# Kernel tuning notes

Hardware: AMD Instinct MI355X
Metric: run time of the kernel (lower is better)

## Reference

```python
import jax, jax.numpy as jnp
import numpy as np

NUM_NODES = 1024
NUM_HEADS = 8
HIDDEN = 256
BOND_DIM = 64
NUM_LAYERS = 3


def _build_edge_index(n):
    # ring + chord graph, both directions -> 4n directed edges, no duplicate (src,tgt) pairs
    u = np.arange(n)
    src = np.concatenate([u, u, (u + 1) % n, (u + 2) % n])
    dst = np.concatenate([(u + 1) % n, (u + 2) % n, u, u])
    return jnp.asarray(np.stack([src, dst]), dtype=jnp.int32)


def setup_inputs() -> dict:
    key = jax.random.key(0)
    ks = jax.random.split(key, 16)
    H, L, B = HIDDEN, NUM_LAYERS, BOND_DIM
    E = 4 * NUM_NODES
    s = 0.02
    inp = {
        "edge_index": _build_edge_index(NUM_NODES),
        "bond_features": jax.random.normal(ks[0], (E, B), jnp.float32),
        # bond_embedding Linear + W_h Linear (stored as [in, out])
        "W_emb": jax.random.normal(ks[1], (B, H), jnp.float32) * s,
        "b_emb": jnp.zeros((H,), jnp.float32),
        "W_h": jax.random.normal(ks[2], (H, H), jnp.float32) * s,
        "b_h": jnp.zeros((H,), jnp.float32),
        # per-layer attention block: pre-LN, qkv in-proj, out-proj
        "ln1_g": jnp.ones((L, H), jnp.float32),
        "ln1_b": jnp.zeros((L, H), jnp.float32),
        "in_w": jax.random.normal(ks[3], (L, H, 3 * H), jnp.float32) * s,
        "in_b": jnp.zeros((L, 3 * H), jnp.float32),
        "out_w": jax.random.normal(ks[4], (L, H, H), jnp.float32) * s,
        "out_b": jnp.zeros((L, H), jnp.float32),
        # per-layer bond_update: Linear -> LayerNorm -> GELU
        "up_w": jax.random.normal(ks[5], (L, H, H), jnp.float32) * s,
        "up_b": jnp.zeros((L, H), jnp.float32),
        "ln2_g": jnp.ones((L, H), jnp.float32),
        "ln2_b": jnp.zeros((L, H), jnp.float32),
    }
    return inp


def _layer_norm(x, g, b, eps=1e-5):
    m = jnp.mean(x, axis=-1, keepdims=True)
    v = jnp.var(x, axis=-1, keepdims=True)
    return (x - m) * jax.lax.rsqrt(v + eps) * g + b


def _mha(x, in_w, in_b, out_w, out_b):
    # x: [E, H]; standard torch MultiheadAttention (batch of 1)
    E, H = x.shape
    d = H // NUM_HEADS
    qkv = x @ in_w + in_b                                  # [E, 3H]
    q, k, v = jnp.split(qkv, 3, axis=-1)
    q = q.reshape(E, NUM_HEADS, d).transpose(1, 0, 2)       # [h, E, d]
    k = k.reshape(E, NUM_HEADS, d).transpose(1, 0, 2)
    v = v.reshape(E, NUM_HEADS, d).transpose(1, 0, 2)
    scores = jnp.einsum("hqd,hkd->hqk", q, k) / jnp.sqrt(jnp.float32(d))
    p = jax.nn.softmax(scores, axis=-1)
    o = jnp.einsum("hqk,hkd->hqd", p, v)                    # [h, E, d]
    o = o.transpose(1, 0, 2).reshape(E, H)
    return o @ out_w + out_b


def _bond_aggregation(edge_index, h):
    # r_e = sum_{e' : tgt(e')=tgt(e), src(e')!=src(e)} (h[e'] - h[e])
    # with no duplicate (src,tgt) pairs this is S[tgt] - deg[tgt] * h
    tgt = edge_index[1]
    S = jax.ops.segment_sum(h, tgt, num_segments=NUM_NODES)                 # [N, H]
    deg = jax.ops.segment_sum(jnp.ones(h.shape[:1], h.dtype), tgt, num_segments=NUM_NODES)
    return S[tgt] - deg[tgt][:, None] * h


def reference(edge_index, bond_features, W_emb, b_emb, W_h, b_h,
              ln1_g, ln1_b, in_w, in_b, out_w, out_b,
              up_w, up_b, ln2_g, ln2_b):
    h = jax.nn.gelu(bond_features @ W_emb + b_emb, approximate=False)
    h = h @ W_h + b_h
    for t in range(NUM_LAYERS):
        r = _bond_aggregation(edge_index, h)
        xn = _layer_norm(r, ln1_g[t], ln1_b[t])
        attn = _mha(xn, in_w[t], in_b[t], out_w[t], out_b[t])
        # block output = attn + r (residual inside block), forward adds + r again
        t_ij = attn + r + r
        u = t_ij @ up_w[t] + up_b[t]
        h = jax.nn.gelu(_layer_norm(u, ln2_g[t], ln2_b[t]), approximate=False)
    return h
```

## Files before the change

### kernel.cpp

```cpp
#include <hip/hip_runtime.h>
#include <hip/hip_bf16.h>
#include <math.h>

#define N_NODES 1024
#define NE      4096
#define HDIM    256
#define QSCALE  0.2550348634f

typedef __hip_bfloat16 bf16;
typedef __attribute__((ext_vector_type(8))) short bf16x8;
typedef __attribute__((ext_vector_type(4))) float f32x4;

__device__ __forceinline__ float u2f(unsigned short u) {
  return __uint_as_float(((unsigned)u) << 16);
}
__device__ __forceinline__ short f2bs(float x) {
  unsigned u = __float_as_uint(x);
  unsigned r = u + 0x7FFFu + ((u >> 16) & 1u);
  return (short)(r >> 16);
}
__device__ __forceinline__ float gelu_f(float x) {
  return 0.5f * x * (1.0f + erff(x * 0.70710678118654752f));
}
__device__ __forceinline__ short rdbf(const void* p, int i, int flag) {
  return flag ? ((const short*)p)[i] : f2bs(((const float*)p)[i]);
}
__device__ __forceinline__ float fexp2(float x) {
#if __has_builtin(__builtin_amdgcn_exp2f)
  return __builtin_amdgcn_exp2f(x);
#else
  return exp2f(x);
#endif
}
__device__ __forceinline__ unsigned pk2(float lo, float hi) {
  return (__float_as_uint(hi) & 0xFFFF0000u) | (__float_as_uint(lo) >> 16);
}
__device__ __forceinline__ unsigned pk2r(float lo, float hi) {
  return (unsigned)(unsigned short)f2bs(lo) |
         ((unsigned)(unsigned short)f2bs(hi) << 16);
}

__global__ __launch_bounds__(64) void k_detect(const unsigned* __restrict__ w,
                                               int* __restrict__ flag) {
  int t = threadIdx.x;
  int cnt = 0;
  for (int i = 0; i < 16; ++i) {
    unsigned v = w[t * 16 + i];
    unsigned e = (v >> 7) & 0xFFu;
    cnt += (e >= 100u && e <= 132u) ? 1 : 0;
  }
#pragma unroll
  for (int k = 1; k < 64; k <<= 1) cnt += __shfl_xor(cnt, k, 64);
  if (t == 0) *flag = (cnt > 512) ? 1 : 0;
}

struct WPtrs { const void* w_emb; const void* w_h; const void* in_w;
               const void* out_w; const void* up_w; };
__global__ __launch_bounds__(256) void k_prep_w(WPtrs a, short* __restrict__ Wt,
                                                const int* __restrict__ flag) {
  int i = blockIdx.x * 256 + threadIdx.x;
  if (i >= 1064960) return;
  const int fl = *flag;
  if (i < 16384) {
    int k = i >> 8, n = i & 255;
    Wt[n * 64 + k] = rdbf(a.w_emb, i, fl);
  } else if (i < 81920) {
    int j = i - 16384;
    int k = j >> 8, n = j & 255;
    Wt[16384 + n * 256 + k] = rdbf(a.w_h, j, fl);
  } else if (i < 671744) {
    int j = i - 81920;
    int t = j / 196608, jj = j % 196608;
    int k = jj / 768, n = jj % 768;
    Wt[81920 + t * 196608 + n * 256 + k] = rdbf(a.in_w, j, fl);
  } else if (i < 868352) {
    int j = i - 671744;
    int t = j >> 16, jj = j & 65535;
    int k = jj >> 8, n = jj & 255;
    Wt[671744 + t * 65536 + n * 256 + k] = rdbf(a.out_w, j, fl);
  } else {
    int j = i - 868352;
    int t = j >> 16, jj = j & 65535;
    int k = jj >> 8, n = jj & 255;
    Wt[868352 + t * 65536 + n * 256 + k] = rdbf(a.up_w, j, fl);
  }
}

struct PPtrs { const void* p[9]; };
__global__ __launch_bounds__(256) void k_cvt_small(PPtrs a, float* __restrict__ dst,
                                                   const int* __restrict__ flag) {
  const int sz[9] = {256, 256, 768, 768, 2304, 768, 768, 768, 768};
  int i = blockIdx.x * 256 + threadIdx.x;
  if (i >= 7424) return;
  int seg = 0, off = i;
  while (off >= sz[seg]) { off -= sz[seg]; ++seg; }
  dst[i] = *flag ? u2f(((const unsigned short*)a.p[seg])[off])
                 : ((const float*)a.p[seg])[off];
}

__global__ __launch_bounds__(256) void k_build_inv(const int* __restrict__ tgt,
                                                   int* __restrict__ cnt,
                                                   int* __restrict__ inv) {
  int e = blockIdx.x * 256 + threadIdx.x;
  if (e < NE) {
    int t = tgt[e];
    int s = atomicAdd(&cnt[t], 1);
    if (s < 8) inv[t * 8 + s] = e;
  }
}

template <int K, bool RAW, bool GELU, bool RES, bool WF, bool WB>
__global__ __launch_bounds__(256) void k_mgemm(const short* __restrict__ A,
                                               const short* __restrict__ Bt,
                                               const float* __restrict__ bias,
                                               const float* __restrict__ res,
                                               float* __restrict__ outF,
                                               short* __restrict__ outB,
                                               const int* __restrict__ flag,
                                               int M, int N) {
  __shared__ alignas(16) short As[64 * K];
  __shared__ alignas(16) short Bs[64 * K];
  const int tid = threadIdx.x;
  const int wave = tid >> 6, lane = tid & 63;
  const int m = lane & 15, quad = lane >> 4;
  const int bm = blockIdx.x * 64, bn = blockIdx.y * 64;
  const int m0 = (wave & 1) * 32, n0 = (wave >> 1) * 32;

  constexpr int CPR = K >> 3;
  constexpr int CPT = K >> 5;

  const int fl = RAW ? *flag : 1;

  int4 ra[CPT], rb[CPT];
#pragma unroll
  for (int i = 0; i < CPT; ++i) {
    const int c = tid + (i << 8);
    const int row = c / CPR, kc = c % CPR;
    if (RAW && !fl) {
      const float* af = (const float*)A + (size_t)(bm + row) * K + kc * 8;
      unsigned* vu = (unsigned*)&ra[i];
      vu[0] = pk2r(af[0], af[1]);
      vu[1] = pk2r(af[2], af[3]);
      vu[2] = pk2r(af[4], af[5]);
      vu[3] = pk2r(af[6], af[7]);
    } else {
      ra[i] = *(const int4*)(A + (size_t)(bm + row) * K + kc * 8);
    }
    rb[i] = *(const int4*)(Bt + (size_t)(bn + row) * K + kc * 8);
  }
#pragma unroll
  for (int i = 0; i < CPT; ++i) {
    const int c = tid + (i << 8);
    const int row = c / CPR, kc = c % CPR;
    *(int4*)&As[row * K + ((kc ^ (row & 7)) << 3)] = ra[i];
    *(int4*)&Bs[row * K + ((kc ^ (row & 7)) << 3)] = rb[i];
  }
  __syncthreads();

  f32x4 acc[2][2];
  acc[0][0] = acc[0][1] = acc[1][0] = acc[1][1] = (f32x4){0.f, 0.f, 0.f, 0.f};

  const int sw = m & 7;
#pragma unroll
  for (int ks = 0; ks < K / 32; ++ks) {
    const int ca = ((ks * 4 + quad) ^ sw) << 3;
    bf16x8 a0 = *(const bf16x8*)&As[(m0 + m) * K + ca];
    bf16x8 a1 = *(const bf16x8*)&As[(m0 + 16 + m) * K + ca];
    bf16x8 b0 = *(const bf16x8*)&Bs[(n0 + m) * K + ca];
    bf16x8 b1 = *(const bf16x8*)&Bs[(n0 + 16 + m) * K + ca];
    acc[0][0] = __builtin_amdgcn_mfma_f32_16x16x32_bf16(a0, b0, acc[0][0], 0, 0, 0);
    acc[0][1] = __builtin_amdgcn_mfma_f32_16x16x32_bf16(a0, b1, acc[0][1], 0, 0, 0);
    acc[1][0] = __builtin_amdgcn_mfma_f32_16x16x32_bf16(a1, b0, acc[1][0], 0, 0, 0);
    acc[1][1] = __builtin_amdgcn_mfma_f32_16x16x32_bf16(a1, b1, acc[1][1], 0, 0, 0);
  }

#pragma unroll
  for (int i = 0; i < 2; ++i)
#pragma unroll
    for (int j = 0; j < 2; ++j) {
      const int col = bn + n0 + j * 16 + m;
      const float bv = bias[col];
#pragma unroll
      for (int r = 0; r < 4; ++r) {
        const int row = bm + m0 + i * 16 + quad * 4 + r;
        float v = acc[i][j][r] + bv;
        if (GELU) v = gelu_f(v);
        if (RES) v += 2.0f * res[(size_t)row * N + col];
        if (WF) outF[(size_t)row * N + col] = v;
        if (WB) outB[(size_t)row * N + col] = f2bs(v);
      }
    }
}

__global__ __launch_bounds__(256) void k_mgemm_out(const short* __restrict__ Opart,
                                                   const float* __restrict__ lpart,
                                                   const short* __restrict__ Bt,
                                                   const float* __restrict__ bias,
                                                   const float* __restrict__ res,
                                                   short* __restrict__ outB) {
  constexpr int K = 256;
  __shared__ alignas(16) short As[64 * K];
  __shared__ alignas(16) short Bs[64 * K];
  const int tid = threadIdx.x;
  const int wave = tid >> 6, lane = tid & 63;
  const int m = lane & 15, quad = lane >> 4;
  const int bm = blockIdx.x * 64, bn = blockIdx.y * 64;
  const int m0 = (wave & 1) * 32, n0 = (wave >> 1) * 32;

  int4 ra[8], rb[8];
#pragma unroll
  for (int i = 0; i < 8; ++i) {
    const int c = tid + (i << 8);
    const int row = c >> 5, kc = c & 31;
    const int R = bm + row, head = kc >> 2;
    float o[8] = {0.f, 0.f, 0.f, 0.f, 0.f, 0.f, 0.f, 0.f};
    float l = 0.f;
#pragma unroll
    for (int s = 0; s < 4; ++s) {
      int4 ov = *(const int4*)(Opart + (size_t)s * 1048576 + (size_t)R * 256 + kc * 8);
      const unsigned short* os = (const unsigned short*)&ov;
#pragma unroll
      for (int j = 0; j < 8; ++j) o[j] += u2f(os[j]);
      l += lpart[(size_t)(s * 8 + head) * 4096 + R];
    }
    const float inv = 1.0f / l;
    unsigned* vu = (unsigned*)&ra[i];
    vu[0] = pk2r(o[0] * inv, o[1] * inv);
    vu[1] = pk2r(o[2] * inv, o[3] * inv);
    vu[2] = pk2r(o[4] * inv, o[5] * inv);
    vu[3] = pk2r(o[6] * inv, o[7] * inv);
    rb[i] = *(const int4*)(Bt + (size_t)(bn + row) * K + kc * 8);
  }
#pragma unroll
  for (int i = 0; i < 8; ++i) {
    const int c = tid + (i << 8);
    const int row = c >> 5, kc = c & 31;
    *(int4*)&As[row * K + ((kc ^ (row & 7)) << 3)] = ra[i];
    *(int4*)&Bs[row * K + ((kc ^ (row & 7)) << 3)] = rb[i];
  }
  __syncthreads();

  f32x4 acc[2][2];
  acc[0][0] = acc[0][1] = acc[1][0] = acc[1][1] = (f32x4){0.f, 0.f, 0.f, 0.f};

  const int sw = m & 7;
#pragma unroll
  for (int ks = 0; ks < K / 32; ++ks) {
    const int ca = ((ks * 4 + quad) ^ sw) << 3;
    bf16x8 a0 = *(const bf16x8*)&As[(m0 + m) * K + ca];
    bf16x8 a1 = *(const bf16x8*)&As[(m0 + 16 + m) * K + ca];
    bf16x8 b0 = *(const bf16x8*)&Bs[(n0 + m) * K + ca];
    bf16x8 b1 = *(const bf16x8*)&Bs[(n0 + 16 + m) * K + ca];
    acc[0][0] = __builtin_amdgcn_mfma_f32_16x16x32_bf16(a0, b0, acc[0][0], 0, 0, 0);
    acc[0][1] = __builtin_amdgcn_mfma_f32_16x16x32_bf16(a0, b1, acc[0][1], 0, 0, 0);
    acc[1][0] = __builtin_amdgcn_mfma_f32_16x16x32_bf16(a1, b0, acc[1][0], 0, 0, 0);
    acc[1][1] = __builtin_amdgcn_mfma_f32_16x16x32_bf16(a1, b1, acc[1][1], 0, 0, 0);
  }

#pragma unroll
  for (int i = 0; i < 2; ++i)
#pragma unroll
    for (int j = 0; j < 2; ++j) {
      const int col = bn + n0 + j * 16 + m;
      const float bv = bias[col];
#pragma unroll
      for (int r = 0; r < 4; ++r) {
        const int row = bm + m0 + i * 16 + quad * 4 + r;
        float v = acc[i][j][r] + bv + 2.0f * res[(size_t)row * 256 + col];
        outB[(size_t)row * 256 + col] = f2bs(v);
      }
    }
}

__global__ __launch_bounds__(256) void k_mgemm_qkv(const short* __restrict__ A,
                                                   const short* __restrict__ Bt,
                                                   const float* __restrict__ bias,
                                                   short* __restrict__ Qh,
                                                   short* __restrict__ Kh,
                                                   short* __restrict__ Vt) {
  constexpr int K = 256;
  __shared__ alignas(16) short As[64 * K];
  __shared__ alignas(16) short Bs[64 * K];
  const int tid = threadIdx.x;
  const int wave = tid >> 6, lane = tid & 63;
  const int m = lane & 15, quad = lane >> 4;
  const int bm = blockIdx.x * 64, bn = blockIdx.y * 64;
  const int m0 = (wave & 1) * 32, n0 = (wave >> 1) * 32;

  int4 ra[8], rb[8];
#pragma unroll
  for (int i = 0; i < 8; ++i) {
    const int c = tid + (i << 8);
    const int row = c >> 5, kc = c & 31;
    ra[i] = *(const int4*)(A + (size_t)(bm + row) * K + kc * 8);
    rb[i] = *(const int4*)(Bt + (size_t)(bn + row) * K + kc * 8);
  }
#pragma unroll
  for (int i = 0; i < 8; ++i) {
    const int c = tid + (i << 8);
    const int row = c >> 5, kc = c & 31;
    *(int4*)&As[row * K + ((kc ^ (row & 7)) << 3)] = ra[i];
    *(int4*)&Bs[row * K + ((kc ^ (row & 7)) << 3)] = rb[i];
  }
  __syncthreads();

  f32x4 acc[2][2];
  acc[0][0] = acc[0][1] = acc[1][0] = acc[1][1] = (f32x4){0.f, 0.f, 0.f, 0.f};

  const int sw = m & 7;
#pragma unroll
  for (int ks = 0; ks < K / 32; ++ks) {
    const int ca = ((ks * 4 + quad) ^ sw) << 3;
    bf16x8 a0 = *(const bf16x8*)&As[(m0 + m) * K + ca];
    bf16x8 a1 = *(const bf16x8*)&As[(m0 + 16 + m) * K + ca];
    bf16x8 b0 = *(const bf16x8*)&Bs[(n0 + m) * K + ca];
    bf16x8 b1 = *(const bf16x8*)&Bs[(n0 + 16 + m) * K + ca];
    acc[0][0] = __builtin_amdgcn_mfma_f32_16x16x32_bf16(a0, b0, acc[0][0], 0, 0, 0);
    acc[0][1] = __builtin_amdgcn_mfma_f32_16x16x32_bf16(a0, b1, acc[0][1], 0, 0, 0);
    acc[1][0] = __builtin_amdgcn_mfma_f32_16x16x32_bf16(a1, b0, acc[1][0], 0, 0, 0);
    acc[1][1] = __builtin_amdgcn_mfma_f32_16x16x32_bf16(a1, b1, acc[1][1], 0, 0, 0);
  }

#pragma unroll
  for (int i = 0; i < 2; ++i)
#pragma unroll
    for (int j = 0; j < 2; ++j) {
      const int col = bn + n0 + j * 16 + m;
      const float bv = bias[col];
      const int row0 = bm + m0 + i * 16 + quad * 4;
      if (col < 256) {
        const int head = col >> 5, d = col & 31;
#pragma unroll
        for (int r = 0; r < 4; ++r)
          Qh[(size_t)head * 131072 + (row0 + r) * 32 + d] =
              f2bs((acc[i][j][r] + bv) * QSCALE);
      } else if (col < 512) {
        const int c = col - 256, head = c >> 5, d = c & 31;
#pragma unroll
        for (int r = 0; r < 4; ++r)
          Kh[(size_t)head * 131072 + (row0 + r) * 32 + d] = f2bs(acc[i][j][r] + bv);
      } else {
        const int c = col - 512, head = c >> 5, d = c & 31;
        const int p0 = (row0 & ~63) + ((row0 >> 5) & 1) * 32 +
                       ((row0 >> 2) & 3) * 8 + ((row0 >> 4) & 1) * 4;
        ushort4 w;
        w.x = (unsigned short)f2bs(acc[i][j][0] + bv);
        w.y = (unsigned short)f2bs(acc[i][j][1] + bv);
        w.z = (unsigned short)f2bs(acc[i][j][2] + bv);
        w.w = (unsigned short)f2bs(acc[i][j][3] + bv);
        *(ushort4*)(Vt + (size_t)head * 131072 + d * 4096 + p0) = w;
      }
    }
}

__global__ __launch_bounds__(256) void k_rln2(const int* __restrict__ tgt,
                                              const int* __restrict__ cnt,
                                              const int* __restrict__ inv,
                                              const float* __restrict__ h,
                                              const float* __restrict__ g,
                                              const float* __restrict__ b,
                                              float* __restrict__ r,
                                              short* __restrict__ xnb) {
  __shared__ float red1[4], red2[4];
  const int e = blockIdx.x, d = threadIdx.x;
  const int t = tgt[e];
  const int c = cnt[t];
  float S = 0.f;
  for (int j = 0; j < c; ++j)
    S += h[(size_t)inv[t * 8 + j] * HDIM + d];
  float rv = S - (float)c * h[(size_t)e * HDIM + d];
  r[(size_t)e * HDIM + d] = rv;

  float s = rv;
#pragma unroll
  for (int k = 1; k < 64; k <<= 1) s += __shfl_xor(s, k, 64);
  if ((d & 63) == 0) red1[d >> 6] = s;
  __syncthreads();
  float mean = (red1[0] + red1[1] + red1[2] + red1[3]) * (1.0f / HDIM);
  float diff = rv - mean;
  float sq = diff * diff;
#pragma unroll
  for (int k = 1; k < 64; k <<= 1) sq += __shfl_xor(sq, k, 64);
  if ((d & 63) == 0) red2[d >> 6] = sq;
  __syncthreads();
  float var = (red2[0] + red2[1] + red2[2] + red2[3]) * (1.0f / HDIM);
  xnb[(size_t)e * HDIM + d] = f2bs(diff * rsqrtf(var + 1e-5f) * g[d] + b[d]);
}

__global__ __launch_bounds__(256) void k_ln_gelu(const float* __restrict__ u,
                                                 const float* __restrict__ g,
                                                 const float* __restrict__ b,
                                                 float* __restrict__ hout,
                                                 void* __restrict__ finalout,
                                                 const int* __restrict__ flag) {
  __shared__ float red1[4], red2[4];
  const int e = blockIdx.x, d = threadIdx.x;
  float v = u[(size_t)e * HDIM + d];
  float s = v;
#pragma unroll
  for (int k = 1; k < 64; k <<= 1) s += __shfl_xor(s, k, 64);
  if ((d & 63) == 0) red1[d >> 6] = s;
  __syncthreads();
  float mean = (red1[0] + red1[1] + red1[2] + red1[3]) * (1.0f / HDIM);
  float diff = v - mean;
  float sq = diff * diff;
#pragma unroll
  for (int k = 1; k < 64; k <<= 1) sq += __shfl_xor(sq, k, 64);
  if ((d & 63) == 0) red2[d >> 6] = sq;
  __syncthreads();
  float var = (red2[0] + red2[1] + red2[2] + red2[3]) * (1.0f / HDIM);
  float xh = diff * rsqrtf(var + 1e-5f) * g[d] + b[d];
  float out = gelu_f(xh);
  hout[(size_t)e * HDIM + d] = out;
  if (finalout) {
    if (*flag)
      ((bf16*)finalout)[(size_t)e * HDIM + d] = __float2bfloat16(out);
    else
      ((float*)finalout)[(size_t)e * HDIM + d] = out;
  }
}

__global__ __launch_bounds__(256) void k_flash4(const short* __restrict__ Qh,
                                                const short* __restrict__ Kh,
                                                const short* __restrict__ Vt,
                                                short* __restrict__ Opart,
                                                float* __restrict__ lpart) {
  __shared__ alignas(16) short Ks[64 * 40];
  __shared__ alignas(16) short Vs[32 * 70 + 8];
  const int head = blockIdx.y, split = blockIdx.z;
  const int tid = threadIdx.x;
  const int wave = tid >> 6, lane = tid & 63;
  const int m = lane & 15, quad = lane >> 4;
  const int q0 = blockIdx.x * 256 + wave * 64;

  const short* Qb = Qh + (size_t)head * 131072;
  const short* Kb = Kh + (size_t)head * 131072;
  const short* Vb = Vt + (size_t)head * 131072;

  bf16x8 qf[4];
#pragma unroll
  for (int a = 0; a < 4; ++a)
    qf[a] = *(const bf16x8*)(Qb + (q0 + a * 16 + m) * 32 + quad * 8);

  f32x4 O[4][2];
  f32x4 lacc[4];
#pragma unroll
  for (int a = 0; a < 4; ++a) {
    O[a][0] = O[a][1] = (f32x4){0.f, 0.f, 0.f, 0.f};
    lacc[a] = (f32x4){0.f, 0.f, 0.f, 0.f};
  }

  bf16x8 ones;
#pragma unroll
  for (int i = 0; i < 8; ++i) ones[i] = (short)0x3F80;

  const int base = split * 1024;
  const int krow = tid >> 2, ko = (tid & 3) * 8;
  const int vrow = tid >> 3, vo = (tid & 7) * 8;
  const short* kstage = Kb + (size_t)(base + krow) * 32 + ko;
  const short* vstage = Vb + (size_t)vrow * 4096 + base + vo;

  int4 rk = *(const int4*)(kstage);
  int4 rv = *(const int4*)(vstage);

#pragma unroll 1
  for (int kb = 0; kb < 16; ++kb) {
    __syncthreads();
    *(int4*)&Ks[krow * 40 + ko] = rk;
    *(int4*)&Vs[vrow * 70 + vo] = rv;
    __syncthreads();
    if (kb < 15) {
      rk = *(const int4*)(kstage + (kb + 1) * 2048);
      rv = *(const int4*)(vstage + (kb + 1) * 64);
    }

    bf16x8 kc0 = *(const bf16x8*)&Ks[(0 * 16 + m) * 40 + quad * 8];
    bf16x8 kc1 = *(const bf16x8*)&Ks[(1 * 16 + m) * 40 + quad * 8];
    bf16x8 kc2 = *(const bf16x8*)&Ks[(2 * 16 + m) * 40 + quad * 8];
    bf16x8 kc3 = *(const bf16x8*)&Ks[(3 * 16 + m) * 40 + quad * 8];
    bf16x8 vc0 = *(const bf16x8*)&Vs[m * 70 + quad * 8];
    bf16x8 vc1 = *(const bf16x8*)&Vs[(m + 16) * 70 + quad * 8];
    bf16x8 vc2 = *(const bf16x8*)&Vs[m * 70 + 32 + quad * 8];
    bf16x8 vc3 = *(const bf16x8*)&Vs[(m + 16) * 70 + 32 + quad * 8];

    const f32x4 z = {0.f, 0.f, 0.f, 0.f};
#pragma unroll
    for (int a = 0; a < 4; ++a) {
      f32x4 S0 = __builtin_amdgcn_mfma_f32_16x16x32_bf16(kc0, qf[a], z, 0, 0, 0);
      f32x4 S1 = __builtin_amdgcn_mfma_f32_16x16x32_bf16(kc1, qf[a], z, 0, 0, 0);
      f32x4 S2 = __builtin_amdgcn_mfma_f32_16x16x32_bf16(kc2, qf[a], z, 0, 0, 0);
      f32x4 S3 = __builtin_amdgcn_mfma_f32_16x16x32_bf16(kc3, qf[a], z, 0, 0, 0);

      float e0[4], e1[4], e2[4], e3[4];
#pragma unroll
      for (int r = 0; r < 4; ++r) {
        e0[r] = fexp2(S0[r]);
        e1[r] = fexp2(S1[r]);
        e2[r] = fexp2(S2[r]);
        e3[r] = fexp2(S3[r]);
      }
      union { bf16x8 v; unsigned u[4]; } pf0, pf1;
      pf0.u[0] = pk2(e0[0], e0[1]);
      pf0.u[1] = pk2(e0[2], e0[3]);
      pf0.u[2] = pk2(e1[0], e1[1]);
      pf0.u[3] = pk2(e1[2], e1[3]);
      pf1.u[0] = pk2(e2[0], e2[1]);
      pf1.u[1] = pk2(e2[2], e2[3]);
      pf1.u[2] = pk2(e3[0], e3[1]);
      pf1.u[3] = pk2(e3[2], e3[3]);

      O[a][0] = __builtin_amdgcn_mfma_f32_16x16x32_bf16(pf0.v, vc0, O[a][0], 0, 0, 0);
      O[a][1] = __builtin_amdgcn_mfma_f32_16x16x32_bf16(pf0.v, vc1, O[a][1], 0, 0, 0);
      lacc[a] = __builtin_amdgcn_mfma_f32_16x16x32_bf16(pf0.v, ones, lacc[a], 0, 0, 0);
      O[a][0] = __builtin_amdgcn_mfma_f32_16x16x32_bf16(pf1.v, vc2, O[a][0], 0, 0, 0);
      O[a][1] = __builtin_amdgcn_mfma_f32_16x16x32_bf16(pf1.v, vc3, O[a][1], 0, 0, 0);
      lacc[a] = __builtin_amdgcn_mfma_f32_16x16x32_bf16(pf1.v, ones, lacc[a], 0, 0, 0);
    }
  }

#pragma unroll
  for (int a = 0; a < 4; ++a)
#pragma unroll
    for (int r = 0; r < 4; ++r) {
      const int row = q0 + a * 16 + quad * 4 + r;
      short* op = Opart + ((size_t)split * 4096 + row) * 256 + head * 32 + m;
      op[0]  = f2bs(O[a][0][r]);
      op[16] = f2bs(O[a][1][r]);
      if (m == 0) lpart[(size_t)(split * 8 + head) * 4096 + row] = lacc[a][r];
    }
}

extern "C" void kernel_launch(void* const* d_in, const int* in_sizes, int n_in,
                              void* d_out, int out_size, void* d_ws, size_t ws_size,
                              hipStream_t stream) {
  const int* edge = (const int*)d_in[0];
  const int* tgt = edge + NE;

  float* ws = (float*)d_ws;
  float* hbuf   = ws;
  float* rbuf   = ws + 1048576;
  int* cnt      = (int*)(ws + 2097152);
  int* inv      = cnt + 1024;
  float* prm    = ws + 2360320;
  short* xn_bf  = (short*)(ws + 2367744);
  short* t_bf   = (short*)(ws + 2892032);
  short* Wt     = (short*)(ws + 3416320);
  short* Qh     = (short*)(ws + 3948800);
  short* Kh     = (short*)(ws + 4473088);
  short* Vt     = (short*)(ws + 4997376);
  float* lpart  = ws + 5521664;
  float* BIG    = ws + 5652736;
  int* flag     = (int*)(ws + 9847040);

  short* e1_bf   = (short*)(BIG + 131072);
  short* Opart   = (short*)BIG;
  float* ubuf    = BIG + 524288;

  const short* Wt_emb = Wt;
  const short* Wt_h   = Wt + 16384;
  const short* Wt_in  = Wt + 81920;
  const short* Wt_out = Wt + 671744;
  const short* Wt_up  = Wt + 868352;
  const float* b_emb = prm;
  const float* b_h   = prm + 256;
  const float* ln1_g = prm + 512;
  const float* ln1_b = prm + 1280;
  const float* in_b  = prm + 2048;
  const float* out_b = prm + 4352;
  const float* up_b  = prm + 5120;
  const float* ln2_g = prm + 5888;
  const float* ln2_b = prm + 6656;

  k_detect<<<dim3(1), dim3(64), 0, stream>>>((const unsigned*)d_in[2], flag);
  WPtrs wp = {d_in[2], d_in[4], d_in[8], d_in[10], d_in[12]};
  k_prep_w<<<dim3(4160), dim3(256), 0, stream>>>(wp, Wt, flag);
  PPtrs pp = {{d_in[3], d_in[5], d_in[6], d_in[7], d_in[9], d_in[11],
               d_in[13], d_in[14], d_in[15]}};
  k_cvt_small<<<dim3(29), dim3(256), 0, stream>>>(pp, prm, flag);
  hipMemsetAsync(cnt, 0, N_NODES * sizeof(int), stream);
  k_build_inv<<<dim3(16), dim3(256), 0, stream>>>(tgt, cnt, inv);

  dim3 blk(256);
  dim3 g256(64, 4);
  dim3 g768(64, 12);
  dim3 gfa(16, 8, 4);

  k_mgemm<64, true, true, false, false, true><<<g256, blk, 0, stream>>>(
      (const short*)d_in[1], Wt_emb, b_emb, nullptr, nullptr, e1_bf, flag,
      NE, 256);
  k_mgemm<256, false, false, false, true, false><<<g256, blk, 0, stream>>>(
      e1_bf, Wt_h, b_h, nullptr, hbuf, nullptr, nullptr, NE, 256);

  for (int t = 0; t < 3; ++t) {
    k_rln2<<<dim3(NE), blk, 0, stream>>>(tgt, cnt, inv, hbuf,
                                         ln1_g + t * HDIM, ln1_b + t * HDIM,
                                         rbuf, xn_bf);
    k_mgemm_qkv<<<g768, blk, 0, stream>>>(xn_bf, Wt_in + (size_t)t * 196608,
                                          in_b + t * 768, Qh, Kh, Vt);
    k_flash4<<<gfa, blk, 0, stream>>>(Qh, Kh, Vt, Opart, lpart);
    k_mgemm_out<<<g256, blk, 0, stream>>>(Opart, lpart,
                                          Wt_out + (size_t)t * 65536,
                                          out_b + t * 256, rbuf, t_bf);
    k_mgemm<256, false, false, false, true, false><<<g256, blk, 0, stream>>>(
        t_bf, Wt_up + (size_t)t * 65536, up_b + t * 256, nullptr,
        ubuf, nullptr, nullptr, NE, 256);
    k_ln_gelu<<<dim3(NE), blk, 0, stream>>>(ubuf, ln2_g + t * HDIM,
                                            ln2_b + t * HDIM, hbuf,
                                            (t == 2) ? d_out : nullptr, flag);
  }
}
```

Before: 292.5 us.

## Fuse up-projection GEMM with LayerNorm+GELU and merge prep kernels

Replaces the per-layer up-projection GEMM and the separate LayerNorm+GELU kernel with one kernel. Each block computes full 16-row by 256-column output tiles, so the row-wise LayerNorm can be reduced in-register and through shared memory, which removes the intermediate fp32 buffer round trip and one launch per layer. The weight, parameter and inverse-index prep kernels and the memset are folded into a single launch, with counter zeroing moved into the detect kernel. The fused kernel runs only 256 blocks and rereads the whole weight matrix for each block, so it trades parallelism for fewer launches and less memory traffic.

```diff
diff --git a/kernel.cpp b/kernel.cpp
--- a/kernel.cpp
+++ b/kernel.cpp
@@ -41,79 +41,77 @@
 }
 
 __global__ __launch_bounds__(64) void k_detect(const unsigned* __restrict__ w,
-                                               int* __restrict__ flag) {
+                                               int* __restrict__ flag,
+                                               int* __restrict__ cnt) {
   int t = threadIdx.x;
-  int cnt = 0;
+  int c = 0;
   for (int i = 0; i < 16; ++i) {
     unsigned v = w[t * 16 + i];
     unsigned e = (v >> 7) & 0xFFu;
-    cnt += (e >= 100u && e <= 132u) ? 1 : 0;
-  }
-#pragma unroll
-  for (int k = 1; k < 64; k <<= 1) cnt += __shfl_xor(cnt, k, 64);
-  if (t == 0) *flag = (cnt > 512) ? 1 : 0;
+    c += (e >= 100u && e <= 132u) ? 1 : 0;
+  }
+#pragma unroll
+  for (int k = 1; k < 64; k <<= 1) c += __shfl_xor(c, k, 64);
+  if (t == 0) *flag = (c > 512) ? 1 : 0;
+#pragma unroll
+  for (int j = 0; j < 16; ++j) cnt[t * 16 + j] = 0;
 }
 
 struct WPtrs { const void* w_emb; const void* w_h; const void* in_w;
                const void* out_w; const void* up_w; };
-__global__ __launch_bounds__(256) void k_prep_w(WPtrs a, short* __restrict__ Wt,
-                                                const int* __restrict__ flag) {
+struct PPtrs { const void* p[9]; };
+__global__ __launch_bounds__(256) void k_prep(WPtrs a, PPtrs pp,
+                                              const int* __restrict__ tgt,
+                                              short* __restrict__ Wt,
+                                              float* __restrict__ prm,
+                                              int* __restrict__ cnt,
+                                              int* __restrict__ inv,
+                                              const int* __restrict__ flag) {
   int i = blockIdx.x * 256 + threadIdx.x;
-  if (i >= 1064960) return;
   const int fl = *flag;
-  if (i < 16384) {
-    int k = i >> 8, n = i & 255;
-    Wt[n * 64 + k] = rdbf(a.w_emb, i, fl);
-  } else if (i < 81920) {
-    int j = i - 16384;
-    int k = j >> 8, n = j & 255;
-    Wt[16384 + n * 256 + k] = rdbf(a.w_h, j, fl);
-  } else if (i < 671744) {
-    int j = i - 81920;
-    int t = j / 196608, jj = j % 196608;
-    int k = jj / 768, n = jj % 768;
-    Wt[81920 + t * 196608 + n * 256 + k] = rdbf(a.in_w, j, fl);
-  } else if (i < 868352) {
-    int j = i - 671744;
-    int t = j >> 16, jj = j & 65535;
-    int k = jj >> 8, n = jj & 255;
-    Wt[671744 + t * 65536 + n * 256 + k] = rdbf(a.out_w, j, fl);
-  } else {
-    int j = i - 868352;
-    int t = j >> 16, jj = j & 65535;
-    int k = jj >> 8, n = jj & 255;
-    Wt[868352 + t * 65536 + n * 256 + k] = rdbf(a.up_w, j, fl);
-  }
-}
-
-struct PPtrs { const void* p[9]; };
-__global__ __launch_bounds__(256) void k_cvt_small(PPtrs a, float* __restrict__ dst,
-                                                   const int* __restrict__ flag) {
-  const int sz[9] = {256, 256, 768, 768, 2304, 768, 768, 768, 768};
-  int i = blockIdx.x * 256 + threadIdx.x;
-  if (i >= 7424) return;
-  int seg = 0, off = i;
-  while (off >= sz[seg]) { off -= sz[seg]; ++seg; }
-  dst[i] = *flag ? u2f(((const unsigned short*)a.p[seg])[off])
-                 : ((const float*)a.p[seg])[off];
-}
-
-__global__ __launch_bounds__(256) void k_build_inv(const int* __restrict__ tgt,
-                                                   int* __restrict__ cnt,
-                                                   int* __restrict__ inv) {
-  int e = blockIdx.x * 256 + threadIdx.x;
-  if (e < NE) {
+  if (i < 1064960) {
+    if (i < 16384) {
+      int k = i >> 8, n = i & 255;
+      Wt[n * 64 + k] = rdbf(a.w_emb, i, fl);
+    } else if (i < 81920) {
+      int j = i - 16384;
+      int k = j >> 8, n = j & 255;
+      Wt[16384 + n * 256 + k] = rdbf(a.w_h, j, fl);
+    } else if (i < 671744) {
+      int j = i - 81920;
+      int t = j / 196608, jj = j % 196608;
+      int k = jj / 768, n = jj % 768;
+      Wt[81920 + t * 196608 + n * 256 + k] = rdbf(a.in_w, j, fl);
+    } else if (i < 868352) {
+      int j = i - 671744;
+      int t = j >> 16, jj = j & 65535;
+      int k = jj >> 8, n = jj & 255;
+      Wt[671744 + t * 65536 + n * 256 + k] = rdbf(a.out_w, j, fl);
+    } else {
+      int j = i - 868352;
+      int t = j >> 16, jj = j & 65535;
+      int k = jj >> 8, n = jj & 255;
+      Wt[868352 + t * 65536 + n * 256 + k] = rdbf(a.up_w, j, fl);
+    }
+  } else if (i < 1072384) {
+    int j = i - 1064960;
+    const int sz[9] = {256, 256, 768, 768, 2304, 768, 768, 768, 768};
+    int seg = 0, off = j;
+    while (off >= sz[seg]) { off -= sz[seg]; ++seg; }
+    prm[j] = fl ? u2f(((const unsigned short*)pp.p[seg])[off])
+                : ((const float*)pp.p[seg])[off];
+  } else if (i < 1076480) {
+    int e = i - 1072384;
     int t = tgt[e];
     int s = atomicAdd(&cnt[t], 1);
     if (s < 8) inv[t * 8 + s] = e;
   }
 }
 
-template <int K, bool RAW, bool GELU, bool RES, bool WF, bool WB>
+template <int K, bool RAW, bool GELU, bool WF, bool WB>
 __global__ __launch_bounds__(256) void k_mgemm(const short* __restrict__ A,
                                                const short* __restrict__ Bt,
                                                const float* __restrict__ bias,
-                                               const float* __restrict__ res,
                                                float* __restrict__ outF,
                                                short* __restrict__ outB,
                                                const int* __restrict__ flag,
@@ -185,7 +183,6 @@
         const int row = bm + m0 + i * 16 + quad * 4 + r;
         float v = acc[i][j][r] + bv;
         if (GELU) v = gelu_f(v);
-        if (RES) v += 2.0f * res[(size_t)row * N + col];
         if (WF) outF[(size_t)row * N + col] = v;
         if (WB) outB[(size_t)row * N + col] = f2bs(v);
       }
@@ -270,6 +267,141 @@
         outB[(size_t)row * 256 + col] = f2bs(v);
       }
     }
+}
+
+__global__ __launch_bounds__(256) void k_up_ln(const short* __restrict__ A,
+                                               const short* __restrict__ Bt,
+                                               const float* __restrict__ bias,
+                                               const float* __restrict__ g,
+                                               const float* __restrict__ b,
+                                               float* __restrict__ hout,
+                                               void* __restrict__ finalout,
+                                               const int* __restrict__ flag) {
+  constexpr int K = 256;
+  __shared__ alignas(16) short As[16 * K];
+  __shared__ alignas(16) short Bs[64 * K];
+  __shared__ float red1[4][16], red2[4][16];
+  const int tid = threadIdx.x;
+  const int wave = tid >> 6, lane = tid & 63;
+  const int m = lane & 15, quad = lane >> 4;
+  const int bm = blockIdx.x * 16;
+
+  int4 qa[2];
+#pragma unroll
+  for (int i = 0; i < 2; ++i) {
+    const int c = tid + (i << 8);
+    const int row = c >> 5, kc = c & 31;
+    qa[i] = *(const int4*)(A + (size_t)(bm + row) * K + kc * 8);
+  }
+#pragma unroll
+  for (int i = 0; i < 2; ++i) {
+    const int c = tid + (i << 8);
+    const int row = c >> 5, kc = c & 31;
+    *(int4*)&As[row * K + ((kc ^ (row & 7)) << 3)] = qa[i];
+  }
+
+  int4 rb[8];
+#pragma unroll
+  for (int i = 0; i < 8; ++i) {
+    const int c = tid + (i << 8);
+    const int row = c >> 5, kc = c & 31;
+    rb[i] = *(const int4*)(Bt + (size_t)row * K + kc * 8);
+  }
+
+  f32x4 acc[4];
+  acc[0] = acc[1] = acc[2] = acc[3] = (f32x4){0.f, 0.f, 0.f, 0.f};
+  const int sw = m & 7;
+
+#pragma unroll 1
+  for (int bn = 0; bn < 4; ++bn) {
+    if (bn) __syncthreads();
+#pragma unroll
+    for (int i = 0; i < 8; ++i) {
+      const int c = tid + (i << 8);
+      const int row = c >> 5, kc = c & 31;
+      *(int4*)&Bs[row * K + ((kc ^ (row & 7)) << 3)] = rb[i];
+    }
+    __syncthreads();
+    if (bn < 3) {
+#pragma unroll
+      for (int i = 0; i < 8; ++i) {
+        const int c = tid + (i << 8);
+        const int row = c >> 5, kc = c & 31;
+        rb[i] = *(const int4*)(Bt + (size_t)((bn + 1) * 64 + row) * K + kc * 8);
+      }
+    }
+#pragma unroll
+    for (int ks = 0; ks < 8; ++ks) {
+      const int ca = ((ks * 4 + quad) ^ sw) << 3;
+      bf16x8 af = *(const bf16x8*)&As[m * K + ca];
+      bf16x8 bf = *(const bf16x8*)&Bs[(wave * 16 + m) * K + ca];
+      acc[bn] = __builtin_amdgcn_mfma_f32_16x16x32_bf16(af, bf, acc[bn], 0, 0, 0);
+    }
+  }
+
+  float u[4][4];
+#pragma unroll
+  for (int bn = 0; bn < 4; ++bn) {
+    const float bv = bias[bn * 64 + wave * 16 + m];
+#pragma unroll
+    for (int r = 0; r < 4; ++r) u[bn][r] = acc[bn][r] + bv;
+  }
+  float s[4];
+#pragma unroll
+  for (int r = 0; r < 4; ++r)
+    s[r] = (u[0][r] + u[1][r]) + (u[2][r] + u[3][r]);
+#pragma unroll
+  for (int k = 1; k < 16; k <<= 1)
+#pragma unroll
+    for (int r = 0; r < 4; ++r) s[r] += __shfl_xor(s[r], k, 64);
+  if (m == 0)
+#pragma unroll
+    for (int r = 0; r < 4; ++r) red1[wave][quad * 4 + r] = s[r];
+  __syncthreads();
+  float mean[4];
+#pragma unroll
+  for (int r = 0; r < 4; ++r) {
+    const int rr = quad * 4 + r;
+    mean[r] = (red1[0][rr] + red1[1][rr] + red1[2][rr] + red1[3][rr]) *
+              (1.0f / HDIM);
+  }
+  float sq[4];
+#pragma unroll
+  for (int r = 0; r < 4; ++r) {
+    float a0 = u[0][r] - mean[r], a1 = u[1][r] - mean[r];
+    float a2 = u[2][r] - mean[r], a3 = u[3][r] - mean[r];
+    sq[r] = (a0 * a0 + a1 * a1) + (a2 * a2 + a3 * a3);
+  }
+#pragma unroll
+  for (int k = 1; k < 16; k <<= 1)
+#pragma unroll
+    for (int r = 0; r < 4; ++r) sq[r] += __shfl_xor(sq[r], k, 64);
+  if (m == 0)
+#pragma unroll
+    for (int r = 0; r < 4; ++r) red2[wave][quad * 4 + r] = sq[r];
+  __syncthreads();
+  const int fl = finalout ? *flag : 0;
+#pragma unroll
+  for (int r = 0; r < 4; ++r) {
+    const int rr = quad * 4 + r;
+    const float var = (red2[0][rr] + red2[1][rr] + red2[2][rr] + red2[3][rr]) *
+                      (1.0f / HDIM);
+    const float rs = rsqrtf(var + 1e-5f);
+    const int row = bm + rr;
+#pragma unroll
+    for (int bn = 0; bn < 4; ++bn) {
+      const int col = bn * 64 + wave * 16 + m;
+      const float xh = (u[bn][r] - mean[r]) * rs * g[col] + b[col];
+      const float out = gelu_f(xh);
+      hout[(size_t)row * HDIM + col] = out;
+      if (finalout) {
+        if (fl)
+          ((bf16*)finalout)[(size_t)row * HDIM + col] = __float2bfloat16(out);
+        else
+          ((float*)finalout)[(size_t)row * HDIM + col] = out;
+      }
+    }
+  }
 }
 
 __global__ __launch_bounds__(256) void k_mgemm_qkv(const short* __restrict__ A,
@@ -387,39 +519,6 @@
   xnb[(size_t)e * HDIM + d] = f2bs(diff * rsqrtf(var + 1e-5f) * g[d] + b[d]);
 }
 
-__global__ __launch_bounds__(256) void k_ln_gelu(const float* __restrict__ u,
-                                                 const float* __restrict__ g,
-                                                 const float* __restrict__ b,
-                                                 float* __restrict__ hout,
-                                                 void* __restrict__ finalout,
-                                                 const int* __restrict__ flag) {
-  __shared__ float red1[4], red2[4];
-  const int e = blockIdx.x, d = threadIdx.x;
-  float v = u[(size_t)e * HDIM + d];
-  float s = v;
-#pragma unroll
-  for (int k = 1; k < 64; k <<= 1) s += __shfl_xor(s, k, 64);
-  if ((d & 63) == 0) red1[d >> 6] = s;
-  __syncthreads();
-  float mean = (red1[0] + red1[1] + red1[2] + red1[3]) * (1.0f / HDIM);
-  float diff = v - mean;
-  float sq = diff * diff;
-#pragma unroll
-  for (int k = 1; k < 64; k <<= 1) sq += __shfl_xor(sq, k, 64);
-  if ((d & 63) == 0) red2[d >> 6] = sq;
-  __syncthreads();
-  float var = (red2[0] + red2[1] + red2[2] + red2[3]) * (1.0f / HDIM);
-  float xh = diff * rsqrtf(var + 1e-5f) * g[d] + b[d];
-  float out = gelu_f(xh);
-  hout[(size_t)e * HDIM + d] = out;
-  if (finalout) {
-    if (*flag)
-      ((bf16*)finalout)[(size_t)e * HDIM + d] = __float2bfloat16(out);
-    else
-      ((float*)finalout)[(size_t)e * HDIM + d] = out;
-  }
-}
-
 __global__ __launch_bounds__(256) void k_flash4(const short* __restrict__ Qh,
                                                 const short* __restrict__ Kh,
                                                 const short* __restrict__ Vt,
@@ -554,7 +653,6 @@
 
   short* e1_bf   = (short*)(BIG + 131072);
   short* Opart   = (short*)BIG;
-  float* ubuf    = BIG + 524288;
 
   const short* Wt_emb = Wt;
   const short* Wt_h   = Wt + 16384;
@@ -571,25 +669,22 @@
   const float* ln2_g = prm + 5888;
   const float* ln2_b = prm + 6656;
 
-  k_detect<<<dim3(1), dim3(64), 0, stream>>>((const unsigned*)d_in[2], flag);
+  k_detect<<<dim3(1), dim3(64), 0, stream>>>((const unsigned*)d_in[2], flag, cnt);
   WPtrs wp = {d_in[2], d_in[4], d_in[8], d_in[10], d_in[12]};
-  k_prep_w<<<dim3(4160), dim3(256), 0, stream>>>(wp, Wt, flag);
   PPtrs pp = {{d_in[3], d_in[5], d_in[6], d_in[7], d_in[9], d_in[11],
                d_in[13], d_in[14], d_in[15]}};
-  k_cvt_small<<<dim3(29), dim3(256), 0, stream>>>(pp, prm, flag);
-  hipMemsetAsync(cnt, 0, N_NODES * sizeof(int), stream);
-  k_build_inv<<<dim3(16), dim3(256), 0, stream>>>(tgt, cnt, inv);
+  k_prep<<<dim3(4205), dim3(256), 0, stream>>>(wp, pp, tgt, Wt, prm, cnt, inv,
+                                               flag);
 
   dim3 blk(256);
   dim3 g256(64, 4);
   dim3 g768(64, 12);
   dim3 gfa(16, 8, 4);
 
-  k_mgemm<64, true, true, false, false, true><<<g256, blk, 0, stream>>>(
-      (const short*)d_in[1], Wt_emb, b_emb, nullptr, nullptr, e1_bf, flag,
-      NE, 256);
-  k_mgemm<256, false, false, false, true, false><<<g256, blk, 0, stream>>>(
-      e1_bf, Wt_h, b_h, nullptr, hbuf, nullptr, nullptr, NE, 256);
+  k_mgemm<64, true, true, false, true><<<g256, blk, 0, stream>>>(
+      (const short*)d_in[1], Wt_emb, b_emb, nullptr, e1_bf, flag, NE, 256);
+  k_mgemm<256, false, false, true, false><<<g256, blk, 0, stream>>>(
+      e1_bf, Wt_h, b_h, hbuf, nullptr, nullptr, NE, 256);
 
   for (int t = 0; t < 3; ++t) {
     k_rln2<<<dim3(NE), blk, 0, stream>>>(tgt, cnt, inv, hbuf,
@@ -601,11 +696,9 @@
     k_mgemm_out<<<g256, blk, 0, stream>>>(Opart, lpart,
                                           Wt_out + (size_t)t * 65536,
                                           out_b + t * 256, rbuf, t_bf);
-    k_mgemm<256, false, false, false, true, false><<<g256, blk, 0, stream>>>(
-        t_bf, Wt_up + (size_t)t * 65536, up_b + t * 256, nullptr,
-        ubuf, nullptr, nullptr, NE, 256);
-    k_ln_gelu<<<dim3(NE), blk, 0, stream>>>(ubuf, ln2_g + t * HDIM,
-                                            ln2_b + t * HDIM, hbuf,
-                                            (t == 2) ? d_out : nullptr, flag);
-  }
-}
+    k_up_ln<<<dim3(256), blk, 0, stream>>>(t_bf, Wt_up + (size_t)t * 65536,
+                                           up_b + t * 256, ln2_g + t * HDIM,
+                                           ln2_b + t * HDIM, hbuf,
+                                           (t == 2) ? d_out : nullptr, flag);
+  }
+}
```

Measured after the change: 314.1 us. 7.4% more time.
